# Optimization experiments

Measured on AMD Instinct MI355X. Metric: run time of the kernel, lower is better.

Reference implementation:

```python
import jax, jax.numpy as jnp
import numpy as np

B, S, H = 2, 2048, 4096          # batch, seq_len, hidden_size
NH, NKV, D = 32, 8, 128          # query heads, kv heads (GQA), head_dim
WINDOW = 1024                    # sliding window size
EPS = 1e-5
THETA = 10000.0


def setup_inputs() -> dict:
    key = jax.random.key(0)
    ks = jax.random.split(key, 5)
    w = lambda k, shape: jax.random.normal(k, shape, jnp.float32) * 0.02
    return {
        "hidden_states": jax.random.normal(ks[0], (B, S, H), jnp.float32),
        "wq": w(ks[1], (H, NH * D)),
        "wk": w(ks[2], (H, NKV * D)),
        "wv": w(ks[3], (H, NKV * D)),
        "wo": w(ks[4], (NH * D, H)),
        "q_norm_w": jnp.ones((D,), jnp.float32),
        "k_norm_w": jnp.ones((D,), jnp.float32),
    }


def _rmsnorm(x, w):
    # Exaone4RMSNorm over the last (head_dim) axis
    var = jnp.mean(jnp.square(x.astype(jnp.float32)), axis=-1, keepdims=True)
    return (x * jax.lax.rsqrt(var + EPS)).astype(x.dtype) * w


def _rotate_half(x):
    x1, x2 = jnp.split(x, 2, axis=-1)
    return jnp.concatenate([-x2, x1], axis=-1)


def reference(hidden_states, wq, wk, wv, wo, q_norm_w, k_norm_w):
    # QKV projections (no bias)
    q = (hidden_states @ wq).reshape(B, S, NH, D)
    k = (hidden_states @ wk).reshape(B, S, NKV, D)
    v = (hidden_states @ wv).reshape(B, S, NKV, D)
    # per-head QK RMSNorm, then [B, h, S, D] layout
    q = _rmsnorm(q, q_norm_w).transpose(0, 2, 1, 3)
    k = _rmsnorm(k, k_norm_w).transpose(0, 2, 1, 3)
    v = v.transpose(0, 2, 1, 3)
    # RoPE (applied on sliding-window layers in EXAONE4)
    pos = jnp.arange(S)
    inv_freq = 1.0 / (THETA ** (jnp.arange(0, D, 2, dtype=jnp.float32) / D))
    freqs = pos[:, None].astype(jnp.float32) * inv_freq[None, :]   # [S, D/2]
    emb = jnp.concatenate([freqs, freqs], axis=-1)                 # [S, D]
    cos, sin = jnp.cos(emb), jnp.sin(emb)
    q = q * cos + _rotate_half(q) * sin
    k = k * cos + _rotate_half(k) * sin
    # GQA: repeat kv heads to match query heads
    k = jnp.repeat(k, NH // NKV, axis=1)
    v = jnp.repeat(v, NH // NKV, axis=1)
    # SDPA with causal sliding-window mask: q_pos - WINDOW < k_pos <= q_pos
    scores = jnp.einsum('bhqd,bhkd->bhqk', q, k) / jnp.sqrt(jnp.float32(D))
    diff = pos[:, None] - pos[None, :]
    mask = (diff >= 0) & (diff < WINDOW)
    scores = jnp.where(mask, scores, jnp.finfo(scores.dtype).min)
    probs = jax.nn.softmax(scores, axis=-1)
    out = jnp.einsum('bhqk,bhkd->bhqd', probs, v)
    out = out.transpose(0, 2, 1, 3).reshape(B, S, NH * D)
    return out @ wo
```

## Files before the change

kernel.cpp:

```cpp
#include <hip/hip_runtime.h>
#include <hip/hip_bf16.h>

#define B_ 2
#define S_ 2048
#define H_ 4096
#define NH_ 32
#define NKV_ 8
#define D_ 128
#define WINDOW_ 1024
#define EPS_ 1e-5f
#define M_ (B_*S_)
#define NQKV_ ((NH_ + 2*NKV_) * D_)

typedef __attribute__((ext_vector_type(8))) __bf16 bf16x8;
typedef __attribute__((ext_vector_type(4))) float f32x4;
typedef __attribute__((ext_vector_type(16))) float f32x16;

__device__ __forceinline__ unsigned short f2bf(float f) {
  union { __hip_bfloat16 h; unsigned short us; } cv;
  cv.h = __float2bfloat16(f);
  return cv.us;
}
__device__ __forceinline__ float bf2f(unsigned short u) {
  union { __hip_bfloat16 h; unsigned short us; } cv;
  cv.us = u;
  return __bfloat162float(cv.h);
}

__device__ __forceinline__ void gload16(const unsigned short* g, unsigned short* l) {
  __builtin_amdgcn_global_load_lds(
      (const __attribute__((address_space(1))) unsigned int*)(const void*)g,
      (__attribute__((address_space(3))) unsigned int*)(void*)l, 16, 0, 0);
}

__global__ __launch_bounds__(256) void transpose_convert(
    const float* __restrict__ in, unsigned short* __restrict__ out, int K, int N) {
  __shared__ unsigned short t[64][72];
  const int n0 = blockIdx.x * 64, k0 = blockIdx.y * 64;
  const int tid = threadIdx.x;
  const int rr = tid >> 4, cc = (tid & 15) * 4;
  #pragma unroll
  for (int i = 0; i < 4; ++i) {
    const int r = i * 16 + rr;
    float4 v = *(const float4*)&in[(size_t)(k0 + r) * N + n0 + cc];
    t[cc + 0][r] = f2bf(v.x);
    t[cc + 1][r] = f2bf(v.y);
    t[cc + 2][r] = f2bf(v.z);
    t[cc + 3][r] = f2bf(v.w);
  }
  __syncthreads();
  #pragma unroll
  for (int i = 0; i < 4; ++i) {
    const int r = i * 16 + rr;
    ushort4 o;
    o.x = t[r][cc + 0]; o.y = t[r][cc + 1];
    o.z = t[r][cc + 2]; o.w = t[r][cc + 3];
    *(ushort4*)&out[(size_t)(n0 + r) * K + k0 + cc] = o;
  }
}

__global__ __launch_bounds__(256) void convert_bf16_kernel(
    const float* __restrict__ in, unsigned short* __restrict__ out, int n4) {
  int i = blockIdx.x * 256 + threadIdx.x;
  if (i >= n4) return;
  float4 v = ((const float4*)in)[i];
  ushort4 o;
  o.x = f2bf(v.x); o.y = f2bf(v.y); o.z = f2bf(v.z); o.w = f2bf(v.w);
  ((ushort4*)out)[i] = o;
}

template <bool OUT_BF16>
__global__ __launch_bounds__(512) void gemm12(
    const unsigned short* __restrict__ A, const unsigned short* __restrict__ Bt,
    void* __restrict__ Cout, int N, int K) {
  __shared__ __align__(16) unsigned short lds[2][28672];
  const int tid = threadIdx.x;
  const int wave = tid >> 6, lane = tid & 63;
  const int l15 = lane & 15, l16 = lane >> 4;
  const int m0 = blockIdx.y * 256, n0 = blockIdx.x * 192;
  const int wmi = wave >> 2, wni = wave & 3;

  const unsigned short* asrc[4];
  const unsigned short* bsrc[3];
  #pragma unroll
  for (int it = 0; it < 4; ++it) {
    const int d = it * 512 + tid;
    const int row = d >> 3, cis = (d & 7) ^ (row & 7);
    asrc[it] = A + (size_t)(m0 + row) * K + cis * 8;
  }
  #pragma unroll
  for (int it = 0; it < 3; ++it) {
    const int d = it * 512 + tid;
    const int row = d >> 3, cis = (d & 7) ^ (row & 7);
    bsrc[it] = Bt + (size_t)(n0 + row) * K + cis * 8;
  }

  int offA[2][8], offB[2][3];
  #pragma unroll
  for (int kk = 0; kk < 2; ++kk) {
    #pragma unroll
    for (int mi = 0; mi < 8; ++mi) {
      const int row = wmi * 128 + mi * 16 + l15;
      offA[kk][mi] = row * 64 + ((kk * 4 + l16) ^ (row & 7)) * 8;
    }
    #pragma unroll
    for (int ni = 0; ni < 3; ++ni) {
      const int row = wni * 48 + ni * 16 + l15;
      offB[kk][ni] = 16384 + row * 64 + ((kk * 4 + l16) ^ (row & 7)) * 8;
    }
  }

  f32x4 acc[8][3];
  #pragma unroll
  for (int mi = 0; mi < 8; ++mi)
    #pragma unroll
    for (int ni = 0; ni < 3; ++ni) acc[mi][ni] = (f32x4){0.f, 0.f, 0.f, 0.f};

#define PHASE_MFMA(MOFF)                                                     \
  asm volatile("s_waitcnt lgkmcnt(0)" ::: "memory");                         \
  __builtin_amdgcn_sched_barrier(0);                                         \
  __builtin_amdgcn_s_setprio(1);                                             \
  _Pragma("unroll") for (int i = 0; i < 4; ++i)                              \
    _Pragma("unroll") for (int j = 0; j < 3; ++j)                            \
      acc[(MOFF) + i][j] = __builtin_amdgcn_mfma_f32_16x16x32_bf16(          \
          av[i], bv[j], acc[(MOFF) + i][j], 0, 0, 0);                        \
  __builtin_amdgcn_s_setprio(0);                                             \
  __builtin_amdgcn_sched_barrier(0);

  #pragma unroll
  for (int it = 0; it < 4; ++it)
    gload16(asrc[it], &lds[0][it * 4096 + wave * 512]);
  #pragma unroll
  for (int it = 0; it < 3; ++it)
    gload16(bsrc[it], &lds[0][16384 + it * 4096 + wave * 512]);
  asm volatile("s_waitcnt vmcnt(0)" ::: "memory");
  __builtin_amdgcn_sched_barrier(0);
  __builtin_amdgcn_s_barrier();

  const int nk = K >> 6;
  for (int t = 0; t < nk; ++t) {
    const int cur = t & 1, nxt = cur ^ 1;
    const unsigned short* ldc = lds[cur];
    const bool dostg = (t + 1 < nk);
    const size_t ko = (size_t)(t + 1) * 64;
    bf16x8 av[4], bv[3];

    #pragma unroll
    for (int i = 0; i < 4; ++i) av[i] = *(const bf16x8*)&ldc[offA[0][i]];
    #pragma unroll
    for (int j = 0; j < 3; ++j) bv[j] = *(const bf16x8*)&ldc[offB[0][j]];
    if (dostg) {
      gload16(asrc[0] + ko, &lds[nxt][0 * 4096 + wave * 512]);
      gload16(asrc[1] + ko, &lds[nxt][1 * 4096 + wave * 512]);
    }
    __builtin_amdgcn_sched_barrier(0);
    __builtin_amdgcn_s_barrier();
    PHASE_MFMA(0)
    __builtin_amdgcn_s_barrier();

    #pragma unroll
    for (int i = 0; i < 4; ++i) av[i] = *(const bf16x8*)&ldc[offA[0][i + 4]];
    if (dostg) {
      gload16(asrc[2] + ko, &lds[nxt][2 * 4096 + wave * 512]);
      gload16(asrc[3] + ko, &lds[nxt][3 * 4096 + wave * 512]);
    }
    __builtin_amdgcn_sched_barrier(0);
    __builtin_amdgcn_s_barrier();
    PHASE_MFMA(4)
    __builtin_amdgcn_s_barrier();

    #pragma unroll
    for (int i = 0; i < 4; ++i) av[i] = *(const bf16x8*)&ldc[offA[1][i]];
    #pragma unroll
    for (int j = 0; j < 3; ++j) bv[j] = *(const bf16x8*)&ldc[offB[1][j]];
    if (dostg) {
      gload16(bsrc[0] + ko, &lds[nxt][16384 + 0 * 4096 + wave * 512]);
      gload16(bsrc[1] + ko, &lds[nxt][16384 + 1 * 4096 + wave * 512]);
    }
    __builtin_amdgcn_sched_barrier(0);
    __builtin_amdgcn_s_barrier();
    PHASE_MFMA(0)
    __builtin_amdgcn_s_barrier();

    #pragma unroll
    for (int i = 0; i < 4; ++i) av[i] = *(const bf16x8*)&ldc[offA[1][i + 4]];
    if (dostg) {
      gload16(bsrc[2] + ko, &lds[nxt][16384 + 2 * 4096 + wave * 512]);
    }
    __builtin_amdgcn_sched_barrier(0);
    __builtin_amdgcn_s_barrier();
    PHASE_MFMA(4)
    asm volatile("s_waitcnt vmcnt(0)" ::: "memory");
    __builtin_amdgcn_sched_barrier(0);
    __builtin_amdgcn_s_barrier();
  }
#undef PHASE_MFMA

  #pragma unroll
  for (int mi = 0; mi < 8; ++mi) {
    #pragma unroll
    for (int ni = 0; ni < 3; ++ni) {
      const int col = n0 + wni * 48 + ni * 16 + l15;
      #pragma unroll
      for (int j = 0; j < 4; ++j) {
        const int row = m0 + wmi * 128 + mi * 16 + l16 * 4 + j;
        if (OUT_BF16)
          ((unsigned short*)Cout)[(size_t)row * N + col] = f2bf(acc[mi][ni][j]);
        else
          ((float*)Cout)[(size_t)row * N + col] = acc[mi][ni][j];
      }
    }
  }
}

template <bool OUT_BF16>
__global__ __launch_bounds__(512) void gemm10(
    const unsigned short* __restrict__ A, const unsigned short* __restrict__ Bt,
    void* __restrict__ Cout, int N, int K) {
  __shared__ __align__(16) unsigned short lds[2][2][16384];
  const int tid = threadIdx.x;
  const int wave = tid >> 6, lane = tid & 63;
  const int l15 = lane & 15, l16 = lane >> 4;
  const int m0 = blockIdx.y * 256, n0 = blockIdx.x * 256;
  const int wmi = wave >> 2, wni = wave & 3;

  const unsigned short* asrc[4];
  const unsigned short* bsrc[4];
  #pragma unroll
  for (int it = 0; it < 4; ++it) {
    const int d = it * 512 + tid;
    const int row = d >> 3, cis = (d & 7) ^ (row & 7);
    asrc[it] = A + (size_t)(m0 + row) * K + cis * 8;
    bsrc[it] = Bt + (size_t)(n0 + row) * K + cis * 8;
  }

  int offA[2][8], offB[2][4];
  #pragma unroll
  for (int kk = 0; kk < 2; ++kk) {
    #pragma unroll
    for (int mi = 0; mi < 8; ++mi) {
      const int row = wmi * 128 + mi * 16 + l15;
      offA[kk][mi] = row * 64 + ((kk * 4 + l16) ^ (row & 7)) * 8;
    }
    #pragma unroll
    for (int ni = 0; ni < 4; ++ni) {
      const int row = wni * 64 + ni * 16 + l15;
      offB[kk][ni] = row * 64 + ((kk * 4 + l16) ^ (row & 7)) * 8;
    }
  }

  f32x4 acc[8][4];
  #pragma unroll
  for (int mi = 0; mi < 8; ++mi)
    #pragma unroll
    for (int ni = 0; ni < 4; ++ni) acc[mi][ni] = (f32x4){0.f, 0.f, 0.f, 0.f};

#define PHASE_MFMA(MOFF)                                                     \
  asm volatile("s_waitcnt lgkmcnt(0)" ::: "memory");                         \
  __builtin_amdgcn_sched_barrier(0);                                         \
  __builtin_amdgcn_s_setprio(1);                                             \
  _Pragma("unroll") for (int i = 0; i < 4; ++i)                              \
    _Pragma("unroll") for (int j = 0; j < 4; ++j)                            \
      acc[(MOFF) + i][j] = __builtin_amdgcn_mfma_f32_16x16x32_bf16(          \
          av[i], bv[j], acc[(MOFF) + i][j], 0, 0, 0);                        \
  __builtin_amdgcn_s_setprio(0);                                             \
  __builtin_amdgcn_sched_barrier(0);

  #pragma unroll
  for (int it = 0; it < 4; ++it) {
    gload16(asrc[it], &lds[0][0][it * 4096 + wave * 512]);
    gload16(bsrc[it], &lds[0][1][it * 4096 + wave * 512]);
  }
  asm volatile("s_waitcnt vmcnt(0)" ::: "memory");
  __builtin_amdgcn_sched_barrier(0);
  __builtin_amdgcn_s_barrier();

  const int nk = K >> 6;
  for (int t = 0; t < nk; ++t) {
    const int cur = t & 1, nxt = cur ^ 1;
    const unsigned short* as = lds[cur][0];
    const unsigned short* bs = lds[cur][1];
    const bool dostg = (t + 1 < nk);
    const size_t ko = (size_t)(t + 1) * 64;
    bf16x8 av[4], bv[4];

    #pragma unroll
    for (int i = 0; i < 4; ++i) av[i] = *(const bf16x8*)&as[offA[0][i]];
    #pragma unroll
    for (int j = 0; j < 4; ++j) bv[j] = *(const bf16x8*)&bs[offB[0][j]];
    if (dostg) {
      gload16(asrc[0] + ko, &lds[nxt][0][0 * 4096 + wave * 512]);
      gload16(asrc[1] + ko, &lds[nxt][0][1 * 4096 + wave * 512]);
    }
    __builtin_amdgcn_sched_barrier(0);
    __builtin_amdgcn_s_barrier();
    PHASE_MFMA(0)
    __builtin_amdgcn_s_barrier();

    #pragma unroll
    for (int i = 0; i < 4; ++i) av[i] = *(const bf16x8*)&as[offA[0][i + 4]];
    if (dostg) {
      gload16(asrc[2] + ko, &lds[nxt][0][2 * 4096 + wave * 512]);
      gload16(asrc[3] + ko, &lds[nxt][0][3 * 4096 + wave * 512]);
    }
    __builtin_amdgcn_sched_barrier(0);
    __builtin_amdgcn_s_barrier();
    PHASE_MFMA(4)
    __builtin_amdgcn_s_barrier();

    #pragma unroll
    for (int i = 0; i < 4; ++i) av[i] = *(const bf16x8*)&as[offA[1][i]];
    #pragma unroll
    for (int j = 0; j < 4; ++j) bv[j] = *(const bf16x8*)&bs[offB[1][j]];
    if (dostg) {
      gload16(bsrc[0] + ko, &lds[nxt][1][0 * 4096 + wave * 512]);
      gload16(bsrc[1] + ko, &lds[nxt][1][1 * 4096 + wave * 512]);
    }
    __builtin_amdgcn_sched_barrier(0);
    __builtin_amdgcn_s_barrier();
    PHASE_MFMA(0)
    __builtin_amdgcn_s_barrier();

    #pragma unroll
    for (int i = 0; i < 4; ++i) av[i] = *(const bf16x8*)&as[offA[1][i + 4]];
    if (dostg) {
      gload16(bsrc[2] + ko, &lds[nxt][1][2 * 4096 + wave * 512]);
      gload16(bsrc[3] + ko, &lds[nxt][1][3 * 4096 + wave * 512]);
    }
    __builtin_amdgcn_sched_barrier(0);
    __builtin_amdgcn_s_barrier();
    PHASE_MFMA(4)
    asm volatile("s_waitcnt vmcnt(0)" ::: "memory");
    __builtin_amdgcn_sched_barrier(0);
    __builtin_amdgcn_s_barrier();
  }
#undef PHASE_MFMA

  #pragma unroll
  for (int mi = 0; mi < 8; ++mi) {
    #pragma unroll
    for (int ni = 0; ni < 4; ++ni) {
      const int col = n0 + wni * 64 + ni * 16 + l15;
      #pragma unroll
      for (int j = 0; j < 4; ++j) {
        const int row = m0 + wmi * 128 + mi * 16 + l16 * 4 + j;
        if (OUT_BF16)
          ((unsigned short*)Cout)[(size_t)row * N + col] = f2bf(acc[mi][ni][j]);
        else
          ((float*)Cout)[(size_t)row * N + col] = acc[mi][ni][j];
      }
    }
  }
}

__global__ __launch_bounds__(256) void norm_rope_kernel(
    const unsigned short* __restrict__ QKVg,
    const float* __restrict__ qw, const float* __restrict__ kw,
    unsigned short* __restrict__ Qr, unsigned short* __restrict__ Kr) {
  const int bs = blockIdx.x;
  const int b = bs >> 11, s = bs & (S_ - 1);
  const int wave = threadIdx.x >> 6, lane = threadIdx.x & 63;

  float invf = 1.0f / powf(10000.0f, (float)lane * (1.0f / 64.0f));
  float sn, cs;
  sincosf((float)s * invf, &sn, &cs);

  const unsigned short* row = QKVg + (size_t)bs * NQKV_;
  const float qwa = qw[lane], qwb = qw[lane + 64];
  const float kwa = kw[lane], kwb = kw[lane + 64];
  const float scale = 0.08838834764831845f;

  for (int h = wave; h < NH_; h += 4) {
    float x0 = bf2f(row[h * D_ + lane]);
    float x1 = bf2f(row[h * D_ + 64 + lane]);
    float ss = x0 * x0 + x1 * x1;
    #pragma unroll
    for (int o = 32; o >= 1; o >>= 1) ss += __shfl_xor(ss, o);
    float r = rsqrtf(ss * (1.0f / 128.0f) + EPS_);
    x0 *= r * qwa; x1 *= r * qwb;
    float o0 = (x0 * cs - x1 * sn) * scale;
    float o1 = (x1 * cs + x0 * sn) * scale;
    size_t off = (((size_t)b * NH_ + h) * S_ + s) * D_;
    Qr[off + lane] = f2bf(o0);
    Qr[off + 64 + lane] = f2bf(o1);
  }
  for (int h = wave; h < NKV_; h += 4) {
    float x0 = bf2f(row[NH_ * D_ + h * D_ + lane]);
    float x1 = bf2f(row[NH_ * D_ + h * D_ + 64 + lane]);
    float ss = x0 * x0 + x1 * x1;
    #pragma unroll
    for (int o = 32; o >= 1; o >>= 1) ss += __shfl_xor(ss, o);
    float r = rsqrtf(ss * (1.0f / 128.0f) + EPS_);
    x0 *= r * kwa; x1 *= r * kwb;
    float o0 = x0 * cs - x1 * sn;
    float o1 = x1 * cs + x0 * sn;
    size_t off = (((size_t)b * NKV_ + h) * S_ + s) * D_;
    Kr[off + lane] = f2bf(o0);
    Kr[off + 64 + lane] = f2bf(o1);
  }
}

__global__ __launch_bounds__(256) void vtrans_kernel(
    const unsigned short* __restrict__ QKVg, unsigned short* __restrict__ Vt) {
  __shared__ unsigned short t[64][65];
  const int s0 = blockIdx.x * 64, d0 = blockIdx.y * 64;
  const int bh = blockIdx.z;
  const int b = bh >> 3, hk = bh & 7;
  const int tid = threadIdx.x;
  #pragma unroll
  for (int i = 0; i < 16; ++i) {
    int e = i * 256 + tid; int sr = e >> 6, dc = e & 63;
    t[sr][dc] = QKVg[(size_t)(b * S_ + s0 + sr) * NQKV_ + (NH_ + NKV_) * D_ + hk * D_ + d0 + dc];
  }
  __syncthreads();
  #pragma unroll
  for (int i = 0; i < 16; ++i) {
    int e = i * 256 + tid; int dr = e >> 6, sc = e & 63;
    Vt[((size_t)bh * D_ + d0 + dr) * S_ + s0 + sc] = t[sc][dr];
  }
}

__global__ __launch_bounds__(512) void attn_kernel(
    const unsigned short* __restrict__ Qr, const unsigned short* __restrict__ Kr,
    const unsigned short* __restrict__ Vt, unsigned short* __restrict__ Out) {
  const int q0 = blockIdx.x * 256;
  const int h = blockIdx.y, b = blockIdx.z, hk = h >> 2;
  const int tid = threadIdx.x;
  const int wave = tid >> 6, lane = tid & 63;
  const int l31 = lane & 31, hi = lane >> 5;
  const int qw0 = q0 + wave * 32;
  const int qpos = qw0 + l31;

  __shared__ __align__(16) unsigned short Ks[64 * 128];
  __shared__ __align__(16) unsigned short Vs[128 * 64];

  bf16x8 qf[8];
  {
    const unsigned short* qp = Qr + (((size_t)b * NH_ + h) * S_ + qpos) * D_ + hi * 8;
    #pragma unroll
    for (int ds = 0; ds < 8; ++ds) qf[ds] = *(const bf16x8*)(qp + ds * 16);
  }

  f32x16 o[4];
  #pragma unroll
  for (int i = 0; i < 4; ++i)
    #pragma unroll
    for (int j = 0; j < 16; ++j) o[i][j] = 0.f;
  float mrun = -1e30f, lrun = 0.f;

  const size_t kbase = ((size_t)b * NKV_ + hk) * S_;
  const size_t vbase = ((size_t)b * NKV_ + hk) * D_;

  const int ktlo = (q0 > 1023) ? ((q0 - 1023) & ~63) : 0;
  const int kthi = (q0 + 255) & ~63;
  const int wlo = (qw0 > 1023) ? ((qw0 - 1023) & ~63) : 0;
  const int whi = (qw0 + 31) & ~63;

  for (int kt = ktlo; kt <= kthi; kt += 64) {
    __syncthreads();
    #pragma unroll
    for (int it = 0; it < 2; ++it) {
      const int cb = it * 512 + wave * 64;
      const int c = cb + lane;
      const int rk = c >> 4, sk = c & 15;
      gload16(Kr + (kbase + kt + rk) * D_ + ((sk ^ (rk & 7)) * 8), Ks + (size_t)cb * 8);
      const int rv = c >> 3, sv = c & 7;
      gload16(Vt + (vbase + rv) * S_ + kt + ((sv ^ (rv & 7)) * 8), Vs + (size_t)cb * 8);
    }
    __syncthreads();
    if (kt < wlo || kt > whi) continue;

    f32x16 s0, s1;
    #pragma unroll
    for (int j = 0; j < 16; ++j) { s0[j] = 0.f; s1[j] = 0.f; }
    __builtin_amdgcn_s_setprio(1);
    #pragma unroll
    for (int ds = 0; ds < 8; ++ds) {
      const int g = ((ds * 2 + hi) ^ (l31 & 7)) * 8;
      bf16x8 k0 = *(const bf16x8*)&Ks[l31 * 128 + g];
      bf16x8 k1 = *(const bf16x8*)&Ks[(l31 + 32) * 128 + g];
      s0 = __builtin_amdgcn_mfma_f32_32x32x16_bf16(k0, qf[ds], s0, 0, 0, 0);
      s1 = __builtin_amdgcn_mfma_f32_32x32x16_bf16(k1, qf[ds], s1, 0, 0, 0);
    }
    __builtin_amdgcn_s_setprio(0);

    const bool fullValid = (kt + 63 <= qw0) && (kt >= qw0 - 992);
    if (!fullValid) {
      const int d0 = qpos - kt;
      #pragma unroll
      for (int r = 0; r < 16; ++r) {
        const int koff = (r & 3) + 8 * (r >> 2) + 4 * hi;
        if ((unsigned)(d0 - koff) >= (unsigned)WINDOW_) s0[r] = -1e30f;
        if ((unsigned)(d0 - koff - 32) >= (unsigned)WINDOW_) s1[r] = -1e30f;
      }
    }

    float pm = -1e30f;
    #pragma unroll
    for (int r = 0; r < 16; ++r) pm = fmaxf(pm, fmaxf(s0[r], s1[r]));
    pm = fmaxf(pm, __shfl_xor(pm, 32));
    if (!__all(pm - mrun <= 8.f)) {
      const float mnew = fmaxf(mrun, pm);
      const float scl = __expf(mrun - mnew);
      mrun = mnew;
      lrun *= scl;
      #pragma unroll
      for (int i = 0; i < 4; ++i)
        #pragma unroll
        for (int j = 0; j < 16; ++j) o[i][j] *= scl;
    }
    float ts = 0.f;
    #pragma unroll
    for (int r = 0; r < 16; ++r) {
      s0[r] = __expf(s0[r] - mrun); ts += s0[r];
      s1[r] = __expf(s1[r] - mrun); ts += s1[r];
    }
    ts += __shfl_xor(ts, 32);
    lrun += ts;

    unsigned pw[2][2][4];
    #pragma unroll
    for (int t2 = 0; t2 < 2; ++t2) {
      const f32x16 sv = t2 ? s1 : s0;
      #pragma unroll
      for (int sub = 0; sub < 2; ++sub) {
        const int bs4 = sub * 8;
        unsigned A0 = ((unsigned)f2bf(sv[bs4 + 1]) << 16) | f2bf(sv[bs4 + 0]);
        unsigned A1 = ((unsigned)f2bf(sv[bs4 + 3]) << 16) | f2bf(sv[bs4 + 2]);
        unsigned B0 = ((unsigned)f2bf(sv[bs4 + 5]) << 16) | f2bf(sv[bs4 + 4]);
        unsigned B1 = ((unsigned)f2bf(sv[bs4 + 7]) << 16) | f2bf(sv[bs4 + 6]);
        unsigned sA0 = __shfl_xor(A0, 32), sA1 = __shfl_xor(A1, 32);
        unsigned sB0 = __shfl_xor(B0, 32), sB1 = __shfl_xor(B1, 32);
        pw[t2][sub][0] = hi ? sB0 : A0;
        pw[t2][sub][1] = hi ? sB1 : A1;
        pw[t2][sub][2] = hi ? B0 : sA0;
        pw[t2][sub][3] = hi ? B1 : sA1;
      }
    }

    __builtin_amdgcn_s_setprio(1);
    #pragma unroll
    for (int t2 = 0; t2 < 2; ++t2)
      #pragma unroll
      for (int sub = 0; sub < 2; ++sub) {
        union { unsigned u[4]; bf16x8 v; } pb;
        pb.u[0] = pw[t2][sub][0]; pb.u[1] = pw[t2][sub][1];
        pb.u[2] = pw[t2][sub][2]; pb.u[3] = pw[t2][sub][3];
        #pragma unroll
        for (int dt = 0; dt < 4; ++dt) {
          const int rr = dt * 32 + l31;
          const int g = ((t2 * 4 + sub * 2 + hi) ^ (rr & 7)) * 8;
          bf16x8 vf = *(const bf16x8*)&Vs[rr * 64 + g];
          o[dt] = __builtin_amdgcn_mfma_f32_32x32x16_bf16(vf, pb.v, o[dt], 0, 0, 0);
        }
      }
    __builtin_amdgcn_s_setprio(0);
  }

  const float inv = 1.0f / lrun;
  unsigned short* op = Out + (size_t)(b * S_ + qpos) * (NH_ * D_) + h * D_;
  #pragma unroll
  for (int dt = 0; dt < 4; ++dt)
    #pragma unroll
    for (int g = 0; g < 4; ++g) {
      const int r = g * 4;
      uint2 val;
      val.x = ((unsigned)f2bf(o[dt][r + 1] * inv) << 16) | f2bf(o[dt][r + 0] * inv);
      val.y = ((unsigned)f2bf(o[dt][r + 3] * inv) << 16) | f2bf(o[dt][r + 2] * inv);
      *(uint2*)(op + dt * 32 + 8 * g + 4 * hi) = val;
    }
}

extern "C" void kernel_launch(void* const* d_in, const int* in_sizes, int n_in,
                              void* d_out, int out_size, void* d_ws, size_t ws_size,
                              hipStream_t stream) {
  const float* hidden = (const float*)d_in[0];
  const float* wq = (const float*)d_in[1];
  const float* wk = (const float*)d_in[2];
  const float* wv = (const float*)d_in[3];
  const float* wo = (const float*)d_in[4];
  const float* qw = (const float*)d_in[5];
  const float* kw = (const float*)d_in[6];
  float* out = (float*)d_out;

  char* ws = (char*)d_ws;
  unsigned short* wqkv = (unsigned short*)(ws);
  unsigned short* kr   = (unsigned short*)(ws);
  unsigned short* vt   = (unsigned short*)(ws + ((size_t)8 << 20));
  unsigned short* attn = (unsigned short*)(ws + ((size_t)16 << 20));
  unsigned short* qkvg = (unsigned short*)(ws + ((size_t)48 << 20));
  unsigned short* wot  = (unsigned short*)(ws + ((size_t)48 << 20));
  unsigned short* hb   = (unsigned short*)d_out;
  unsigned short* qr   = (unsigned short*)d_out + ((size_t)16 << 20);

  transpose_convert<<<dim3(NH_ * D_ / 64, H_ / 64), 256, 0, stream>>>(wq, wqkv, H_, NH_ * D_);
  transpose_convert<<<dim3(NKV_ * D_ / 64, H_ / 64), 256, 0, stream>>>(
      wk, wqkv + (size_t)NH_ * D_ * H_, H_, NKV_ * D_);
  transpose_convert<<<dim3(NKV_ * D_ / 64, H_ / 64), 256, 0, stream>>>(
      wv, wqkv + (size_t)(NH_ + NKV_) * D_ * H_, H_, NKV_ * D_);

  convert_bf16_kernel<<<(M_ * H_ / 4 + 255) / 256, 256, 0, stream>>>(hidden, hb, M_ * H_ / 4);

  gemm12<true><<<dim3(NQKV_ / 192, M_ / 256), 512, 0, stream>>>(hb, wqkv, qkvg, NQKV_, H_);

  norm_rope_kernel<<<M_, 256, 0, stream>>>(qkvg, qw, kw, qr, kr);

  vtrans_kernel<<<dim3(S_ / 64, D_ / 64, B_ * NKV_), 256, 0, stream>>>(qkvg, vt);

  transpose_convert<<<dim3(H_ / 64, H_ / 64), 256, 0, stream>>>(wo, wot, NH_ * D_, H_);

  attn_kernel<<<dim3(S_ / 256, NH_, B_), 512, 0, stream>>>(qr, kr, vt, attn);

  gemm10<false><<<dim3(H_ / 256, M_ / 256), 512, 0, stream>>>(attn, wot, out, H_, H_);
}
```

Baseline: 511.7 us.

## Double-buffer K/V tiles in attention kernel to overlap loads with MFMA compute

```diff
diff --git a/kernel.cpp b/kernel.cpp
--- a/kernel.cpp
+++ b/kernel.cpp
@@ -431,8 +431,8 @@
   const int qw0 = q0 + wave * 32;
   const int qpos = qw0 + l31;
 
-  __shared__ __align__(16) unsigned short Ks[64 * 128];
-  __shared__ __align__(16) unsigned short Vs[128 * 64];
+  __shared__ __align__(16) unsigned short Ks[2][64 * 128];
+  __shared__ __align__(16) unsigned short Vs[2][128 * 64];
 
   bf16x8 qf[8];
   {
@@ -456,106 +456,125 @@
   const int wlo = (qw0 > 1023) ? ((qw0 - 1023) & ~63) : 0;
   const int whi = (qw0 + 31) & ~63;
 
+#define STAGE_KV(buf, kt)                                                    \
+  { _Pragma("unroll") for (int it = 0; it < 2; ++it) {                       \
+      const int cb = it * 512 + wave * 64;                                   \
+      const int c = cb + lane;                                               \
+      const int rk = c >> 4, sk = c & 15;                                    \
+      gload16(Kr + (kbase + (kt) + rk) * D_ + ((sk ^ (rk & 7)) * 8),         \
+              &Ks[buf][(size_t)cb * 8]);                                     \
+      const int rv = c >> 3, sv = c & 7;                                     \
+      gload16(Vt + (vbase + rv) * S_ + (kt) + ((sv ^ (rv & 7)) * 8),         \
+              &Vs[buf][(size_t)cb * 8]);                                     \
+    } }
+
+  STAGE_KV(0, ktlo)
+  asm volatile("s_waitcnt vmcnt(0)" ::: "memory");
+  __builtin_amdgcn_sched_barrier(0);
+  __builtin_amdgcn_s_barrier();
+
+  int cur = 0;
   for (int kt = ktlo; kt <= kthi; kt += 64) {
-    __syncthreads();
-    #pragma unroll
-    for (int it = 0; it < 2; ++it) {
-      const int cb = it * 512 + wave * 64;
-      const int c = cb + lane;
-      const int rk = c >> 4, sk = c & 15;
-      gload16(Kr + (kbase + kt + rk) * D_ + ((sk ^ (rk & 7)) * 8), Ks + (size_t)cb * 8);
-      const int rv = c >> 3, sv = c & 7;
-      gload16(Vt + (vbase + rv) * S_ + kt + ((sv ^ (rv & 7)) * 8), Vs + (size_t)cb * 8);
-    }
-    __syncthreads();
-    if (kt < wlo || kt > whi) continue;
-
-    f32x16 s0, s1;
-    #pragma unroll
-    for (int j = 0; j < 16; ++j) { s0[j] = 0.f; s1[j] = 0.f; }
-    __builtin_amdgcn_s_setprio(1);
-    #pragma unroll
-    for (int ds = 0; ds < 8; ++ds) {
-      const int g = ((ds * 2 + hi) ^ (l31 & 7)) * 8;
-      bf16x8 k0 = *(const bf16x8*)&Ks[l31 * 128 + g];
-      bf16x8 k1 = *(const bf16x8*)&Ks[(l31 + 32) * 128 + g];
-      s0 = __builtin_amdgcn_mfma_f32_32x32x16_bf16(k0, qf[ds], s0, 0, 0, 0);
-      s1 = __builtin_amdgcn_mfma_f32_32x32x16_bf16(k1, qf[ds], s1, 0, 0, 0);
-    }
-    __builtin_amdgcn_s_setprio(0);
-
-    const bool fullValid = (kt + 63 <= qw0) && (kt >= qw0 - 992);
-    if (!fullValid) {
-      const int d0 = qpos - kt;
-      #pragma unroll
-      for (int r = 0; r < 16; ++r) {
-        const int koff = (r & 3) + 8 * (r >> 2) + 4 * hi;
-        if ((unsigned)(d0 - koff) >= (unsigned)WINDOW_) s0[r] = -1e30f;
-        if ((unsigned)(d0 - koff - 32) >= (unsigned)WINDOW_) s1[r] = -1e30f;
+    if (kt + 64 <= kthi) STAGE_KV(cur ^ 1, kt + 64)
+    __builtin_amdgcn_sched_barrier(0);
+
+    if (kt >= wlo && kt <= whi) {
+      const unsigned short* ksb = Ks[cur];
+      const unsigned short* vsb = Vs[cur];
+
+      f32x16 s0, s1;
+      #pragma unroll
+      for (int j = 0; j < 16; ++j) { s0[j] = 0.f; s1[j] = 0.f; }
+      __builtin_amdgcn_s_setprio(1);
+      #pragma unroll
+      for (int ds = 0; ds < 8; ++ds) {
+        const int g = ((ds * 2 + hi) ^ (l31 & 7)) * 8;
+        bf16x8 k0 = *(const bf16x8*)&ksb[l31 * 128 + g];
+        bf16x8 k1 = *(const bf16x8*)&ksb[(l31 + 32) * 128 + g];
+        s0 = __builtin_amdgcn_mfma_f32_32x32x16_bf16(k0, qf[ds], s0, 0, 0, 0);
+        s1 = __builtin_amdgcn_mfma_f32_32x32x16_bf16(k1, qf[ds], s1, 0, 0, 0);
       }
-    }
-
-    float pm = -1e30f;
-    #pragma unroll
-    for (int r = 0; r < 16; ++r) pm = fmaxf(pm, fmaxf(s0[r], s1[r]));
-    pm = fmaxf(pm, __shfl_xor(pm, 32));
-    if (!__all(pm - mrun <= 8.f)) {
-      const float mnew = fmaxf(mrun, pm);
-      const float scl = __expf(mrun - mnew);
-      mrun = mnew;
-      lrun *= scl;
-      #pragma unroll
-      for (int i = 0; i < 4; ++i)
+      __builtin_amdgcn_s_setprio(0);
+
+      const bool fullValid = (kt + 63 <= qw0) && (kt >= qw0 - 992);
+      if (!fullValid) {
+        const int d0 = qpos - kt;
         #pragma unroll
-        for (int j = 0; j < 16; ++j) o[i][j] *= scl;
-    }
-    float ts = 0.f;
-    #pragma unroll
-    for (int r = 0; r < 16; ++r) {
-      s0[r] = __expf(s0[r] - mrun); ts += s0[r];
-      s1[r] = __expf(s1[r] - mrun); ts += s1[r];
-    }
-    ts += __shfl_xor(ts, 32);
-    lrun += ts;
-
-    unsigned pw[2][2][4];
-    #pragma unroll
-    for (int t2 = 0; t2 < 2; ++t2) {
-      const f32x16 sv = t2 ? s1 : s0;
-      #pragma unroll
-      for (int sub = 0; sub < 2; ++sub) {
-        const int bs4 = sub * 8;
-        unsigned A0 = ((unsigned)f2bf(sv[bs4 + 1]) << 16) | f2bf(sv[bs4 + 0]);
-        unsigned A1 = ((unsigned)f2bf(sv[bs4 + 3]) << 16) | f2bf(sv[bs4 + 2]);
-        unsigned B0 = ((unsigned)f2bf(sv[bs4 + 5]) << 16) | f2bf(sv[bs4 + 4]);
-        unsigned B1 = ((unsigned)f2bf(sv[bs4 + 7]) << 16) | f2bf(sv[bs4 + 6]);
-        unsigned sA0 = __shfl_xor(A0, 32), sA1 = __shfl_xor(A1, 32);
-        unsigned sB0 = __shfl_xor(B0, 32), sB1 = __shfl_xor(B1, 32);
-        pw[t2][sub][0] = hi ? sB0 : A0;
-        pw[t2][sub][1] = hi ? sB1 : A1;
-        pw[t2][sub][2] = hi ? B0 : sA0;
-        pw[t2][sub][3] = hi ? B1 : sA1;
-      }
-    }
-
-    __builtin_amdgcn_s_setprio(1);
-    #pragma unroll
-    for (int t2 = 0; t2 < 2; ++t2)
-      #pragma unroll
-      for (int sub = 0; sub < 2; ++sub) {
-        union { unsigned u[4]; bf16x8 v; } pb;
-        pb.u[0] = pw[t2][sub][0]; pb.u[1] = pw[t2][sub][1];
-        pb.u[2] = pw[t2][sub][2]; pb.u[3] = pw[t2][sub][3];
-        #pragma unroll
-        for (int dt = 0; dt < 4; ++dt) {
-          const int rr = dt * 32 + l31;
-          const int g = ((t2 * 4 + sub * 2 + hi) ^ (rr & 7)) * 8;
-          bf16x8 vf = *(const bf16x8*)&Vs[rr * 64 + g];
-          o[dt] = __builtin_amdgcn_mfma_f32_32x32x16_bf16(vf, pb.v, o[dt], 0, 0, 0);
+        for (int r = 0; r < 16; ++r) {
+          const int koff = (r & 3) + 8 * (r >> 2) + 4 * hi;
+          if ((unsigned)(d0 - koff) >= (unsigned)WINDOW_) s0[r] = -1e30f;
+          if ((unsigned)(d0 - koff - 32) >= (unsigned)WINDOW_) s1[r] = -1e30f;
         }
       }
-    __builtin_amdgcn_s_setprio(0);
-  }
+
+      float pm = -1e30f;
+      #pragma unroll
+      for (int r = 0; r < 16; ++r) pm = fmaxf(pm, fmaxf(s0[r], s1[r]));
+      pm = fmaxf(pm, __shfl_xor(pm, 32));
+      if (!__all(pm - mrun <= 8.f)) {
+        const float mnew = fmaxf(mrun, pm);
+        const float scl = __expf(mrun - mnew);
+        mrun = mnew;
+        lrun *= scl;
+        #pragma unroll
+        for (int i = 0; i < 4; ++i)
+          #pragma unroll
+          for (int j = 0; j < 16; ++j) o[i][j] *= scl;
+      }
+      float ts = 0.f;
+      #pragma unroll
+      for (int r = 0; r < 16; ++r) {
+        s0[r] = __expf(s0[r] - mrun); ts += s0[r];
+        s1[r] = __expf(s1[r] - mrun); ts += s1[r];
+      }
+      ts += __shfl_xor(ts, 32);
+      lrun += ts;
+
+      unsigned pw[2][2][4];
+      #pragma unroll
+      for (int t2 = 0; t2 < 2; ++t2) {
+        const f32x16 sv = t2 ? s1 : s0;
+        #pragma unroll
+        for (int sub = 0; sub < 2; ++sub) {
+          const int bs4 = sub * 8;
+          unsigned A0 = ((unsigned)f2bf(sv[bs4 + 1]) << 16) | f2bf(sv[bs4 + 0]);
+          unsigned A1 = ((unsigned)f2bf(sv[bs4 + 3]) << 16) | f2bf(sv[bs4 + 2]);
+          unsigned B0 = ((unsigned)f2bf(sv[bs4 + 5]) << 16) | f2bf(sv[bs4 + 4]);
+          unsigned B1 = ((unsigned)f2bf(sv[bs4 + 7]) << 16) | f2bf(sv[bs4 + 6]);
+          unsigned sA0 = __shfl_xor(A0, 32), sA1 = __shfl_xor(A1, 32);
+          unsigned sB0 = __shfl_xor(B0, 32), sB1 = __shfl_xor(B1, 32);
+          pw[t2][sub][0] = hi ? sB0 : A0;
+          pw[t2][sub][1] = hi ? sB1 : A1;
+          pw[t2][sub][2] = hi ? B0 : sA0;
+          pw[t2][sub][3] = hi ? B1 : sA1;
+        }
+      }
+
+      __builtin_amdgcn_s_setprio(1);
+      #pragma unroll
+      for (int t2 = 0; t2 < 2; ++t2)
+        #pragma unroll
+        for (int sub = 0; sub < 2; ++sub) {
+          union { unsigned u[4]; bf16x8 v; } pb;
+          pb.u[0] = pw[t2][sub][0]; pb.u[1] = pw[t2][sub][1];
+          pb.u[2] = pw[t2][sub][2]; pb.u[3] = pw[t2][sub][3];
+          #pragma unroll
+          for (int dt = 0; dt < 4; ++dt) {
+            const int rr = dt * 32 + l31;
+            const int g = ((t2 * 4 + sub * 2 + hi) ^ (rr & 7)) * 8;
+            bf16x8 vf = *(const bf16x8*)&vsb[rr * 64 + g];
+            o[dt] = __builtin_amdgcn_mfma_f32_32x32x16_bf16(vf, pb.v, o[dt], 0, 0, 0);
+          }
+        }
+      __builtin_amdgcn_s_setprio(0);
+    }
+
+    asm volatile("s_waitcnt vmcnt(0)" ::: "memory");
+    __builtin_amdgcn_sched_barrier(0);
+    __builtin_amdgcn_s_barrier();
+    cur ^= 1;
+  }
+#undef STAGE_KV
 
   const float inv = 1.0f / lrun;
   unsigned short* op = Out + (size_t)(b * S_ + qpos) * (NH_ * D_) + h * D_;
```

Result: no change. 513.8 us (+0.4%).
